# Optimization experiments

Measured on AMD Instinct MI355X. Metric: run time of the kernel, lower is better.

## Reference

```python
import jax, jax.numpy as jnp
import numpy as np

AFWD = 0.999   # alpha_fwd
ABKW = 0.99    # alpha_bkw
EPS = 1e-05


def setup_inputs() -> dict:
    key = jax.random.key(0)
    B, H, W, C = 32, 64, 64, 256
    x = jax.random.normal(key, (B, H, W, C), dtype=jnp.float32)
    return {
        "x": x,
        "mu0": jnp.zeros((C,), jnp.float32),   # streaming mean  (zeros init)
        "var0": jnp.ones((C,), jnp.float32),   # streaming var   (ones init)
        "u0": jnp.zeros((C,), jnp.float32),    # u control (bwd) (zeros init)
        "v0": jnp.zeros((C,), jnp.float32),    # v control (bwd) (zeros init)
    }


def _fwd_scan(x, mu0, var0):
    """Online Normalization forward: sequential EMA over the batch axis.

    Per sample t (channels-last, stats per channel over spatial dims):
      out_t   = (x_t - mu_{t-1}) / sqrt(var_{t-1} + eps)
      var_t   = a*var_{t-1} + (1-a)*Var[x_t] + a*(1-a)*(E[x_t]-mu_{t-1})^2
      mu_t    = mu_{t-1} + (1-a)*(E[x_t]-mu_{t-1})
    The TF layer accelerates this same recurrence with afpow/abpow convs.
    """
    def step(carry, xt):                      # xt: [H, W, C]
        s_mu, s_var = carry                   # [C], [C]
        scale = jnp.sqrt(s_var + EPS)         # [C]
        out = (xt - s_mu) / scale             # broadcast over H, W
        mu_t = jnp.mean(xt, axis=(0, 1))                      # [C]
        var_t = jnp.mean(jnp.square(xt - mu_t), axis=(0, 1))  # biased var, [C]
        new_var = AFWD * s_var + (1.0 - AFWD) * var_t \
                  + AFWD * (1.0 - AFWD) * jnp.square(mu_t - s_mu)
        new_mu = s_mu + (1.0 - AFWD) * (mu_t - s_mu)
        return (new_mu, new_var), (out, scale)

    (mu_f, var_f), (out, scale) = jax.lax.scan(step, (mu0, var0), x)
    return out, scale, mu_f, var_f


def reference(x, mu0, var0, u0, v0):
    out, _, _, _ = _fwd_scan(x, mu0, var0)
    return out
```

## Files before the change

kernel.cpp:

```cpp
#include <hip/hip_runtime.h>
#include <math.h>

#define AFWD 0.999f
#define EPS  1e-5f

constexpr int B  = 32;
constexpr int HW = 64 * 64;
constexpr int C  = 256;
constexpr int CQ = C / 4;
constexpr int CHUNKS = 32;
constexpr int RPC = HW / CHUNKS;

__global__ void __launch_bounds__(256)
k1_partial(const float4* __restrict__ x4,
           float* __restrict__ accum_s,
           float* __restrict__ accum_q) {
    const int blk   = blockIdx.x;
    const int t     = blk >> 5;
    const int chunk = blk & 31;
    const int tid   = threadIdx.x;
    const int cq    = tid & 63;
    const int rs    = tid >> 6;

    const long base = (long)(t * HW + chunk * RPC) * CQ;

    float4 s = make_float4(0.f, 0.f, 0.f, 0.f);
    float4 q = make_float4(0.f, 0.f, 0.f, 0.f);
    #pragma unroll 4
    for (int k = 0; k < RPC / 4; ++k) {
        const float4 v = x4[base + (long)(rs + k * 4) * CQ + cq];
        s.x += v.x; s.y += v.y; s.z += v.z; s.w += v.w;
        q.x += v.x * v.x; q.y += v.y * v.y; q.z += v.z * v.z; q.w += v.w * v.w;
    }

    __shared__ float4 ls[256];
    __shared__ float4 lq[256];
    ls[tid] = s;
    lq[tid] = q;
    __syncthreads();

    const int c    = tid;
    const int cq2  = c >> 2;
    const int comp = c & 3;
    float ssum = 0.f, qsum = 0.f;
    #pragma unroll
    for (int k = 0; k < 4; ++k) {
        ssum += ((const float*)&ls[k * 64 + cq2])[comp];
        qsum += ((const float*)&lq[k * 64 + cq2])[comp];
    }
    atomicAdd(&accum_s[t * C + c], ssum);
    atomicAdd(&accum_q[t * C + c], qsum);
}

__global__ void __launch_bounds__(256)
k2_norm(const float4* __restrict__ x4,
        const float* __restrict__ mu0,
        const float* __restrict__ var0,
        const float* __restrict__ accum_s,
        const float* __restrict__ accum_q,
        float4* __restrict__ out4) {
    const int blk   = blockIdx.x;
    const int t     = blk >> 5;
    const int chunk = blk & 31;
    const int tid   = threadIdx.x;

    float mu  = mu0[tid];
    float var = var0[tid];
    const float inv = 1.0f / (float)HW;
    for (int tt = 0; tt < t; ++tt) {
        const float m  = accum_s[tt * C + tid] * inv;
        const float vt = accum_q[tt * C + tid] * inv - m * m;
        const float d  = m - mu;
        var = AFWD * var + (1.0f - AFWD) * vt + AFWD * (1.0f - AFWD) * d * d;
        mu  = mu + (1.0f - AFWD) * d;
    }

    __shared__ float smu[C];
    __shared__ float srs[C];
    smu[tid] = mu;
    srs[tid] = 1.0f / sqrtf(var + EPS);
    __syncthreads();

    const int cq = tid & 63;
    const int rs = tid >> 6;
    const float4 mu4 = ((const float4*)smu)[cq];
    const float4 rs4 = ((const float4*)srs)[cq];

    const long base = (long)(t * HW + chunk * RPC) * CQ;
    #pragma unroll 4
    for (int k = 0; k < RPC / 4; ++k) {
        const long i = base + (long)(rs + k * 4) * CQ + cq;
        const float4 v = x4[i];
        float4 o;
        o.x = (v.x - mu4.x) * rs4.x;
        o.y = (v.y - mu4.y) * rs4.y;
        o.z = (v.z - mu4.z) * rs4.z;
        o.w = (v.w - mu4.w) * rs4.w;
        out4[i] = o;
    }
}

extern "C" void kernel_launch(void* const* d_in, const int* in_sizes, int n_in,
                              void* d_out, int out_size, void* d_ws, size_t ws_size,
                              hipStream_t stream) {
    const float4* x4   = (const float4*)d_in[0];
    const float*  mu0  = (const float*)d_in[1];
    const float*  var0 = (const float*)d_in[2];
    float4* out4 = (float4*)d_out;

    float* accum_s = (float*)d_ws;
    float* accum_q = accum_s + B * C;

    hipMemsetAsync(d_ws, 0, 2 * B * C * sizeof(float), stream);

    k1_partial<<<dim3(B * CHUNKS), 256, 0, stream>>>(x4, accum_s, accum_q);

    k2_norm<<<dim3(B * CHUNKS), 256, 0, stream>>>(x4, mu0, var0,
                                                  accum_s, accum_q, out4);
}
```

Baseline: 263.9 us.

## Fuse stats and normalize into one cooperative persistent kernel with flag sync

Replaces the two-pass design (a stats kernel, then a normalize kernel that re-reads x) with a single cooperative kernel. Each of 512 blocks keeps a 64-row chunk in registers, publishes per-sample partial sums via atomics plus a per-sample done counter, waits for earlier samples, updates the running mean/var, and writes the output with nontemporal stores. This removes the second global read of x (about half the input traffic) and one launch. In exchange it adds spin-wait synchronisation across blocks and serialises the samples within each block's loop, so there is a risk of stalls while blocks wait on each other.

```diff
diff --git a/kernel.cpp b/kernel.cpp
--- a/kernel.cpp
+++ b/kernel.cpp
@@ -4,99 +4,121 @@
 #define AFWD 0.999f
 #define EPS  1e-5f
 
-constexpr int B  = 32;
-constexpr int HW = 64 * 64;
-constexpr int C  = 256;
-constexpr int CQ = C / 4;
-constexpr int CHUNKS = 32;
-constexpr int RPC = HW / CHUNKS;
+constexpr int B      = 32;
+constexpr int HW     = 64 * 64;
+constexpr int C      = 256;
+constexpr int CQ     = C / 4;
+constexpr int R      = 64;
+constexpr int CHUNKS = HW / R;
+constexpr int TG     = 8;
+constexpr int GRID   = TG * CHUNKS;
+constexpr int ITERS  = B / TG;
+constexpr int F4PT   = R / 4;
 
-__global__ void __launch_bounds__(256)
-k1_partial(const float4* __restrict__ x4,
-           float* __restrict__ accum_s,
-           float* __restrict__ accum_q) {
-    const int blk   = blockIdx.x;
-    const int t     = blk >> 5;
-    const int chunk = blk & 31;
+typedef float nfloat4 __attribute__((ext_vector_type(4)));
+
+__global__ void __launch_bounds__(256, 2)
+fused_onorm(const float4* __restrict__ x4,
+            const float*  __restrict__ mu0,
+            const float*  __restrict__ var0,
+            float*        __restrict__ accum_s,
+            float*        __restrict__ accum_q,
+            int*          __restrict__ done,
+            float4*       __restrict__ out4) {
+    const int b     = blockIdx.x;
+    const int tg    = b >> 6;
+    const int chunk = b & 63;
     const int tid   = threadIdx.x;
     const int cq    = tid & 63;
     const int rs    = tid >> 6;
 
-    const long base = (long)(t * HW + chunk * RPC) * CQ;
-
-    float4 s = make_float4(0.f, 0.f, 0.f, 0.f);
-    float4 q = make_float4(0.f, 0.f, 0.f, 0.f);
-    #pragma unroll 4
-    for (int k = 0; k < RPC / 4; ++k) {
-        const float4 v = x4[base + (long)(rs + k * 4) * CQ + cq];
-        s.x += v.x; s.y += v.y; s.z += v.z; s.w += v.w;
-        q.x += v.x * v.x; q.y += v.y * v.y; q.z += v.z * v.z; q.w += v.w * v.w;
-    }
-
     __shared__ float4 ls[256];
     __shared__ float4 lq[256];
-    ls[tid] = s;
-    lq[tid] = q;
-    __syncthreads();
-
-    const int c    = tid;
-    const int cq2  = c >> 2;
-    const int comp = c & 3;
-    float ssum = 0.f, qsum = 0.f;
-    #pragma unroll
-    for (int k = 0; k < 4; ++k) {
-        ssum += ((const float*)&ls[k * 64 + cq2])[comp];
-        qsum += ((const float*)&lq[k * 64 + cq2])[comp];
-    }
-    atomicAdd(&accum_s[t * C + c], ssum);
-    atomicAdd(&accum_q[t * C + c], qsum);
-}
-
-__global__ void __launch_bounds__(256)
-k2_norm(const float4* __restrict__ x4,
-        const float* __restrict__ mu0,
-        const float* __restrict__ var0,
-        const float* __restrict__ accum_s,
-        const float* __restrict__ accum_q,
-        float4* __restrict__ out4) {
-    const int blk   = blockIdx.x;
-    const int t     = blk >> 5;
-    const int chunk = blk & 31;
-    const int tid   = threadIdx.x;
+    __shared__ __align__(16) float smu[C];
+    __shared__ __align__(16) float srs[C];
 
     float mu  = mu0[tid];
     float var = var0[tid];
+    int upto  = 0;
     const float inv = 1.0f / (float)HW;
-    for (int tt = 0; tt < t; ++tt) {
-        const float m  = accum_s[tt * C + tid] * inv;
-        const float vt = accum_q[tt * C + tid] * inv - m * m;
-        const float d  = m - mu;
-        var = AFWD * var + (1.0f - AFWD) * vt + AFWD * (1.0f - AFWD) * d * d;
-        mu  = mu + (1.0f - AFWD) * d;
-    }
 
-    __shared__ float smu[C];
-    __shared__ float srs[C];
-    smu[tid] = mu;
-    srs[tid] = 1.0f / sqrtf(var + EPS);
-    __syncthreads();
+    for (int i = 0; i < ITERS; ++i) {
+        const int t    = i * TG + tg;
+        const int base = (t * HW + chunk * R) * CQ;
 
-    const int cq = tid & 63;
-    const int rs = tid >> 6;
-    const float4 mu4 = ((const float4*)smu)[cq];
-    const float4 rs4 = ((const float4*)srs)[cq];
+        float4 v[F4PT];
+        #pragma unroll
+        for (int k = 0; k < F4PT; ++k)
+            v[k] = x4[base + (rs + k * 4) * CQ + cq];
 
-    const long base = (long)(t * HW + chunk * RPC) * CQ;
-    #pragma unroll 4
-    for (int k = 0; k < RPC / 4; ++k) {
-        const long i = base + (long)(rs + k * 4) * CQ + cq;
-        const float4 v = x4[i];
-        float4 o;
-        o.x = (v.x - mu4.x) * rs4.x;
-        o.y = (v.y - mu4.y) * rs4.y;
-        o.z = (v.z - mu4.z) * rs4.z;
-        o.w = (v.w - mu4.w) * rs4.w;
-        out4[i] = o;
+        float4 s = make_float4(0.f, 0.f, 0.f, 0.f);
+        float4 q = make_float4(0.f, 0.f, 0.f, 0.f);
+        #pragma unroll
+        for (int k = 0; k < F4PT; ++k) {
+            s.x += v[k].x; s.y += v[k].y; s.z += v[k].z; s.w += v[k].w;
+            q.x += v[k].x * v[k].x; q.y += v[k].y * v[k].y;
+            q.z += v[k].z * v[k].z; q.w += v[k].w * v[k].w;
+        }
+
+        ls[tid] = s;
+        lq[tid] = q;
+        __syncthreads();
+        {
+            const int c2 = tid >> 2, comp = tid & 3;
+            float ss = 0.f, qq = 0.f;
+            #pragma unroll
+            for (int k = 0; k < 4; ++k) {
+                ss += ((const float*)&ls[k * 64 + c2])[comp];
+                qq += ((const float*)&lq[k * 64 + c2])[comp];
+            }
+            atomicAdd(&accum_s[t * C + tid], ss);
+            atomicAdd(&accum_q[t * C + tid], qq);
+        }
+        __threadfence();
+        __syncthreads();
+
+        if (tid == 0) {
+            __hip_atomic_fetch_add(&done[t], 1, __ATOMIC_RELEASE,
+                                   __HIP_MEMORY_SCOPE_AGENT);
+            for (int tt = upto; tt < t; ++tt)
+                while (__hip_atomic_load(&done[tt], __ATOMIC_ACQUIRE,
+                                         __HIP_MEMORY_SCOPE_AGENT) < CHUNKS)
+                    __builtin_amdgcn_s_sleep(2);
+        }
+        __syncthreads();
+
+        for (int tt = upto; tt < t; ++tt) {
+            const float S = __hip_atomic_load(&accum_s[tt * C + tid],
+                                              __ATOMIC_RELAXED,
+                                              __HIP_MEMORY_SCOPE_AGENT);
+            const float Q = __hip_atomic_load(&accum_q[tt * C + tid],
+                                              __ATOMIC_RELAXED,
+                                              __HIP_MEMORY_SCOPE_AGENT);
+            const float m  = S * inv;
+            const float vt = Q * inv - m * m;
+            const float d  = m - mu;
+            var = AFWD * var + (1.0f - AFWD) * vt
+                + AFWD * (1.0f - AFWD) * d * d;
+            mu  = mu + (1.0f - AFWD) * d;
+        }
+        upto = t;
+
+        smu[tid] = mu;
+        srs[tid] = 1.0f / sqrtf(var + EPS);
+        __syncthreads();
+
+        const float4 m4 = ((const float4*)smu)[cq];
+        const float4 r4 = ((const float4*)srs)[cq];
+        #pragma unroll
+        for (int k = 0; k < F4PT; ++k) {
+            nfloat4 o;
+            o.x = (v[k].x - m4.x) * r4.x;
+            o.y = (v[k].y - m4.y) * r4.y;
+            o.z = (v[k].z - m4.z) * r4.z;
+            o.w = (v[k].w - m4.w) * r4.w;
+            __builtin_nontemporal_store(
+                o, (nfloat4*)&out4[base + (rs + k * 4) * CQ + cq]);
+        }
     }
 }
 
@@ -110,11 +132,14 @@
 
     float* accum_s = (float*)d_ws;
     float* accum_q = accum_s + B * C;
+    int*   done    = (int*)(accum_q + B * C);
 
-    hipMemsetAsync(d_ws, 0, 2 * B * C * sizeof(float), stream);
+    (void)hipMemsetAsync(d_ws, 0,
+                         (size_t)(2 * B * C) * sizeof(float) + B * sizeof(int),
+                         stream);
 
-    k1_partial<<<dim3(B * CHUNKS), 256, 0, stream>>>(x4, accum_s, accum_q);
-
-    k2_norm<<<dim3(B * CHUNKS), 256, 0, stream>>>(x4, mu0, var0,
-                                                  accum_s, accum_q, out4);
+    void* args[] = {(void*)&x4, (void*)&mu0, (void*)&var0,
+                    (void*)&accum_s, (void*)&accum_q, (void*)&done, (void*)&out4};
+    (void)hipLaunchCooperativeKernel((const void*)fused_onorm, dim3(GRID),
+                                     dim3(256), args, 0, stream);
 }
```

Measured after the change: 773.5 us. 193% more time.
